# Kernel tuning notes

Measured on AMD Instinct MI355X. Metric: run time of the kernel, lower is better.

## Reference

```python
import jax, jax.numpy as jnp
import numpy as np

N_NODES = 100000   # n_user (70k) + m_item (30k)
N_EDGES = 2000000  # bidirectional user-item interaction edges
DIM = 64           # latent_dim = config['recdim']


def setup_inputs() -> dict:
    key = jax.random.key(0)
    k1, k2, k3, k4 = jax.random.split(key, 4)
    x = jax.random.normal(k1, (N_NODES, DIM), dtype=jnp.float32)
    edge_index = jax.random.randint(k2, (2, N_EDGES), 0, N_NODES, dtype=jnp.int32)
    # w_linears: Linear(2*D, D) per layer; stored as [in, out] so y = h @ W + b
    s = 1.0 / np.sqrt(2 * DIM)
    W0 = jax.random.normal(k3, (2 * DIM, DIM), dtype=jnp.float32) * s
    b0 = jnp.zeros((DIM,), dtype=jnp.float32)
    W1 = jax.random.normal(k4, (2 * DIM, DIM), dtype=jnp.float32) * s
    b1 = jnp.zeros((DIM,), dtype=jnp.float32)
    return {"x": x, "edge_index": edge_index, "W0": W0, "b0": b0, "W1": W1, "b1": b1}


def reference(x, edge_index, W0, b0, W1, b1):
    # SAGE-style: neighbor gather + mean aggregation + concat(self, agg) + per-layer linear
    n = x.shape[0]
    src = edge_index[0]  # message source nodes
    dst = edge_index[1]  # message destination nodes
    deg = jax.ops.segment_sum(jnp.ones(src.shape[0], x.dtype), dst, num_segments=n)
    inv_deg = (1.0 / jnp.maximum(deg, 1.0))[:, None]  # [N,1] mean normalizer

    h = x
    layers = ((W0, b0, True), (W1, b1, False))
    for W, b, apply_relu in layers:
        agg = jax.ops.segment_sum(h[src], dst, num_segments=n) * inv_deg  # [N,D] neighbor mean
        h = jnp.concatenate([h, agg], axis=1) @ W + b                      # [N,2D] @ [2D,D]
        if apply_relu:
            h = jax.nn.relu(h)
    return h
```

## Files before the change

### kernel.cpp

```cpp
#include <hip/hip_runtime.h>
#include <hip/hip_bf16.h>

#define N_NODES 100000
#define N_EDGES 2000000
#define DIM 64
#define NB 391
#define CAP 8192
#define PCAP 8192
#define EPB 4096
#define EPT 16
#define BIN_BLOCKS ((N_EDGES + EPB - 1) / EPB)
#define XCONV_BLOCKS (N_NODES * DIM / 4 / 256)

typedef __attribute__((ext_vector_type(8))) short short8;
typedef __attribute__((ext_vector_type(4))) float f32x4;
typedef __attribute__((ext_vector_type(2))) float f32x2;

__global__ __launch_bounds__(256) void binprep_kernel(const int* __restrict__ src,
                                                      const int* __restrict__ dst,
                                                      int* __restrict__ gbcur,
                                                      int* __restrict__ ebuf,
                                                      const float* __restrict__ x,
                                                      uint2* __restrict__ xb4,
                                                      int* __restrict__ xf8,
                                                      const float* __restrict__ W0,
                                                      const float* __restrict__ W1,
                                                      __hip_bfloat16* __restrict__ wfrag) {
    __shared__ int buf[EPB];
    __shared__ short bufb[EPB];
    __shared__ int a[512];
    __shared__ int lscan[NB], lcur[NB], gbase[NB];

    const int bid = blockIdx.x;
    if (bid >= BIN_BLOCKS) {
        const int pb = bid - BIN_BLOCKS;
        if (pb < XCONV_BLOCKS) {
            const int i = pb * 256 + threadIdx.x;
            const float4 v = ((const float4*)x)[i];
            __hip_bfloat162 p0 = __float22bfloat162_rn(make_float2(v.x, v.y));
            __hip_bfloat162 p1 = __float22bfloat162_rn(make_float2(v.z, v.w));
            uint2 ob;
            ob.x = *(unsigned int*)&p0;
            ob.y = *(unsigned int*)&p1;
            xb4[i] = ob;
            int w = __builtin_amdgcn_cvt_pk_fp8_f32(v.x, v.y, 0, false);
            w = __builtin_amdgcn_cvt_pk_fp8_f32(v.z, v.w, w, true);
            xf8[i] = w;
        } else {
            const int tid = (pb - XCONV_BLOCKS) * 256 + threadIdx.x;
            const int j    = tid & 7;
            const int lane = (tid >> 3) & 63;
            const int kc   = (tid >> 9) & 3;
            const int nt   = (tid >> 11) & 3;
            const int l    = tid >> 13;
            const int k = kc * 32 + (lane >> 4) * 8 + j;
            const int n = nt * 16 + (lane & 15);
            const float* W = l ? W1 : W0;
            wfrag[tid] = __float2bfloat16(W[k * 64 + n]);
        }
        return;
    }

    const int t = threadIdx.x;
    const int e0 = bid * EPB;
    const int cnt = min(EPB, N_EDGES - e0);

    for (int i = t; i < 512; i += 256) a[i] = 0;
    __syncthreads();

    int ls[EPT], ld[EPT];
    #pragma unroll
    for (int k = 0; k < EPT; ++k) {
        const int o = t + k * 256;
        if (o < cnt) {
            ls[k] = src[e0 + o];
            ld[k] = dst[e0 + o];
            atomicAdd(&a[ld[k] >> 8], 1);
        } else ld[k] = -1;
    }
    __syncthreads();

    #pragma unroll
    for (int d = 1; d < 512; d <<= 1) {
        const int idx = (t + 1) * 2 * d - 1;
        if (idx < 512) a[idx] += a[idx - d];
        __syncthreads();
    }
    if (t == 0) a[511] = 0;
    __syncthreads();
    #pragma unroll
    for (int d = 256; d >= 1; d >>= 1) {
        const int idx = (t + 1) * 2 * d - 1;
        if (idx < 512) {
            const int tmp = a[idx - d];
            a[idx - d] = a[idx];
            a[idx] += tmp;
        }
        __syncthreads();
    }
    for (int i = t; i < NB; i += 256) {
        const int c = a[i + 1] - a[i];
        lscan[i] = a[i];
        lcur[i]  = a[i];
        gbase[i] = c ? atomicAdd(&gbcur[i], c) : 0;
    }
    __syncthreads();

    #pragma unroll
    for (int k = 0; k < EPT; ++k) {
        if (ld[k] >= 0) {
            const int b = ld[k] >> 8;
            const int p = atomicAdd(&lcur[b], 1);
            buf[p]  = (ls[k] << 8) | (ld[k] & 255);
            bufb[p] = (short)b;
        }
    }
    __syncthreads();
    for (int i = t; i < cnt; i += 256) {
        const int pk = buf[i];
        const int b  = bufb[i];
        ebuf[b * CAP + gbase[b] + (i - lscan[b])] = pk;
    }
}

__global__ __launch_bounds__(256) void fillpass_kernel(const int* __restrict__ ebuf,
                                                       const int* __restrict__ gbcur,
                                                       int2* __restrict__ nodeinfo,
                                                       int* __restrict__ csr) {
    __shared__ int cnt[256];
    __shared__ int s[256];
    __shared__ int cur[256];
    const int b = blockIdx.x;
    const int t = threadIdx.x;
    const int nbase = b << 8;
    const int ecnt = gbcur[b];
    const int estart = b * CAP;

    cnt[t] = 0;
    __syncthreads();
    for (int i = t; i < ecnt; i += 256)
        atomicAdd(&cnt[ebuf[estart + i] & 255], 1);
    __syncthreads();

    const int deg  = cnt[t];
    const int pdeg = (deg + 7) & ~7;
    s[t] = pdeg;
    __syncthreads();
    #pragma unroll
    for (int off = 1; off < 256; off <<= 1) {
        int u = (t >= off) ? s[t - off] : 0;
        __syncthreads();
        s[t] += u;
        __syncthreads();
    }
    const int rp = b * PCAP + s[t] - pdeg;
    if (nbase + t < N_NODES) nodeinfo[nbase + t] = make_int2(rp, deg);
    cur[t] = rp;
    __syncthreads();

    for (int i = t; i < ecnt; i += 256) {
        const int pk = ebuf[estart + i];
        const int p = atomicAdd(&cur[pk & 255], 1);
        csr[p] = pk >> 8;
    }
    __syncthreads();
    for (int p = rp + deg; p < rp + pdeg; ++p)
        csr[p] = N_NODES;
}

__global__ __launch_bounds__(256) void gather_kernel(const uint2* __restrict__ f8tbl,
                                                     const int2* __restrict__ nodeinfo,
                                                     const int* __restrict__ csr,
                                                     uint4* __restrict__ agg16) {
    const int wave = threadIdx.x >> 6;
    const int lane = threadIdx.x & 63;
    const int node = blockIdx.x * 4 + wave;
    const int2 ni = nodeinfo[node];
    const int rp0 = ni.x;
    const int deg = ni.y;
    const int pcnt = (deg + 7) & ~7;
    const int o = lane >> 3;
    const int r = lane & 7;

    float a0 = 0.f, a1 = 0.f, a2 = 0.f, a3 = 0.f;
    float a4 = 0.f, a5 = 0.f, a6 = 0.f, a7 = 0.f;

    #define CONSUME(u)                                                        \
        {                                                                     \
            f32x2 f01 = __builtin_amdgcn_cvt_pk_f32_fp8((u).x, false);        \
            f32x2 f23 = __builtin_amdgcn_cvt_pk_f32_fp8((u).x, true);         \
            f32x2 f45 = __builtin_amdgcn_cvt_pk_f32_fp8((u).y, false);        \
            f32x2 f67 = __builtin_amdgcn_cvt_pk_f32_fp8((u).y, true);         \
            a0 += f01.x; a1 += f01.y; a2 += f23.x; a3 += f23.y;               \
            a4 += f45.x; a5 += f45.y; a6 += f67.x; a7 += f67.y;               \
        }

    for (int base = 0; base < pcnt; base += 64) {
        const int rem = min(pcnt - base, 64);
        const int idx = (lane < rem)
            ? __builtin_nontemporal_load(csr + rp0 + base + lane) : 0;
        int j = 0;
        for (; j + 32 <= rem; j += 32) {
            const int s0 = __shfl(idx, j + o);
            const int s1 = __shfl(idx, j + 8 + o);
            const int s2 = __shfl(idx, j + 16 + o);
            const int s3 = __shfl(idx, j + 24 + o);
            const uint2 u0 = f8tbl[(size_t)s0 * 8 + r];
            const uint2 u1 = f8tbl[(size_t)s1 * 8 + r];
            const uint2 u2 = f8tbl[(size_t)s2 * 8 + r];
            const uint2 u3 = f8tbl[(size_t)s3 * 8 + r];
            CONSUME(u0); CONSUME(u1); CONSUME(u2); CONSUME(u3);
        }
        for (; j < rem; j += 8) {
            const int s = __shfl(idx, j + o);
            const uint2 u = f8tbl[(size_t)s * 8 + r];
            CONSUME(u);
        }
    }
    #undef CONSUME

    #define RED(A) A += __shfl_xor(A, 8); A += __shfl_xor(A, 16); A += __shfl_xor(A, 32);
    RED(a0) RED(a1) RED(a2) RED(a3) RED(a4) RED(a5) RED(a6) RED(a7)
    #undef RED

    if (o == 0) {
        const float inv = 1.0f / fmaxf((float)deg, 1.0f);
        __hip_bfloat162 p0 = __float22bfloat162_rn(make_float2(a0 * inv, a1 * inv));
        __hip_bfloat162 p1 = __float22bfloat162_rn(make_float2(a2 * inv, a3 * inv));
        __hip_bfloat162 p2 = __float22bfloat162_rn(make_float2(a4 * inv, a5 * inv));
        __hip_bfloat162 p3 = __float22bfloat162_rn(make_float2(a6 * inv, a7 * inv));
        uint4 ov;
        ov.x = *(unsigned int*)&p0;
        ov.y = *(unsigned int*)&p1;
        ov.z = *(unsigned int*)&p2;
        ov.w = *(unsigned int*)&p3;
        agg16[(size_t)node * 8 + r] = ov;
    }
}

template <bool RELU, bool OUTF32, bool WRF8>
__global__ __launch_bounds__(256) void gemm_kernel(const unsigned short* __restrict__ hb,
                                                   const unsigned short* __restrict__ aggb,
                                                   const unsigned short* __restrict__ wfrag,
                                                   const float* __restrict__ bias,
                                                   float* __restrict__ outf,
                                                   unsigned short* __restrict__ outb,
                                                   unsigned char* __restrict__ outf8) {
    const int wave = threadIdx.x >> 6;
    const int lane = threadIdx.x & 63;
    const int m0 = (blockIdx.x * 4 + wave) * 16;
    const int quad = lane >> 4;
    const int lrow = lane & 15;
    const int m = min(m0 + lrow, N_NODES - 1);

    short8 bf[4][4];
    #pragma unroll
    for (int nt = 0; nt < 4; ++nt)
        #pragma unroll
        for (int kc = 0; kc < 4; ++kc)
            bf[nt][kc] = *(const short8*)(wfrag + (size_t)((nt * 4 + kc) * 64 + lane) * 8);

    f32x4 acc[4];
    #pragma unroll
    for (int nt = 0; nt < 4; ++nt) acc[nt] = f32x4{0.f, 0.f, 0.f, 0.f};

    #pragma unroll
    for (int kc = 0; kc < 4; ++kc) {
        const unsigned short* ap = (kc < 2)
            ? (hb   + (size_t)m * 64 + kc * 32 + quad * 8)
            : (aggb + (size_t)m * 64 + (kc - 2) * 32 + quad * 8);
        const short8 af = *(const short8*)ap;
        #pragma unroll
        for (int nt = 0; nt < 4; ++nt)
            acc[nt] = __builtin_amdgcn_mfma_f32_16x16x32_bf16(af, bf[nt][kc], acc[nt], 0, 0, 0);
    }

    #pragma unroll
    for (int nt = 0; nt < 4; ++nt) {
        const float bv = bias[nt * 16 + lrow];
        #pragma unroll
        for (int r = 0; r < 4; ++r) {
            const int mr = m0 + quad * 4 + r;
            if (mr < N_NODES) {
                float v = acc[nt][r] + bv;
                if (RELU) v = fmaxf(v, 0.f);
                const size_t off = (size_t)mr * 64 + nt * 16 + lrow;
                if (OUTF32) {
                    outf[off] = v;
                } else {
                    __hip_bfloat16 hv = __float2bfloat16(v);
                    outb[off] = *(unsigned short*)&hv;
                }
                if (WRF8) {
                    const int w8 = __builtin_amdgcn_cvt_pk_fp8_f32(v, v, 0, false);
                    outf8[off] = (unsigned char)(w8 & 0xff);
                }
            }
        }
    }
}

extern "C" void kernel_launch(void* const* d_in, const int* in_sizes, int n_in,
                              void* d_out, int out_size, void* d_ws, size_t ws_size,
                              hipStream_t stream) {
    const float* x  = (const float*)d_in[0];
    const int*   ei = (const int*)d_in[1];
    const float* W0 = (const float*)d_in[2];
    const float* b0 = (const float*)d_in[3];
    const float* W1 = (const float*)d_in[4];
    const float* b1 = (const float*)d_in[5];
    float* out = (float*)d_out;

    const int* src = ei;
    const int* dst = ei + N_EDGES;

    char* ws = (char*)d_ws;
    auto alloc = [&](size_t bytes) {
        char* p = ws;
        ws += (bytes + 255) & ~(size_t)255;
        return p;
    };
    int*  gbcur    = (int*)alloc((size_t)NB * 4);
    int2* nodeinfo = (int2*)alloc((size_t)N_NODES * 8);
    int*  ebuf     = (int*)alloc((size_t)NB * CAP * 4);
    int*  csr      = (int*)alloc((size_t)NB * PCAP * 4);
    unsigned short* xb   = (unsigned short*)alloc((size_t)N_NODES * DIM * 2);
    unsigned char*  xf8  = (unsigned char*)alloc((size_t)(N_NODES + 1) * DIM);
    unsigned short* aggb = (unsigned short*)alloc((size_t)N_NODES * DIM * 2);
    unsigned short* h1b  = (unsigned short*)alloc((size_t)N_NODES * DIM * 2);
    unsigned char*  h1f8 = (unsigned char*)alloc((size_t)(N_NODES + 1) * DIM);
    __hip_bfloat16* wfrag = (__hip_bfloat16*)alloc((size_t)2 * 8192 * 2);

    hipMemsetAsync(gbcur, 0, (size_t)NB * 4, stream);
    hipMemsetAsync(xf8  + (size_t)N_NODES * DIM, 0, DIM, stream);
    hipMemsetAsync(h1f8 + (size_t)N_NODES * DIM, 0, DIM, stream);

    binprep_kernel<<<BIN_BLOCKS + XCONV_BLOCKS + 64, 256, 0, stream>>>(
        src, dst, gbcur, ebuf, x, (uint2*)xb, (int*)xf8, W0, W1, wfrag);
    fillpass_kernel<<<NB, 256, 0, stream>>>(ebuf, gbcur, nodeinfo, csr);

    const int gemm_blocks = (N_NODES + 63) / 64;

    gather_kernel<<<N_NODES / 4, 256, 0, stream>>>((const uint2*)xf8, nodeinfo, csr,
                                                   (uint4*)aggb);
    gemm_kernel<true, false, true><<<gemm_blocks, 256, 0, stream>>>(
        xb, aggb, (const unsigned short*)wfrag, b0, nullptr, h1b, h1f8);

    gather_kernel<<<N_NODES / 4, 256, 0, stream>>>((const uint2*)h1f8, nodeinfo, csr,
                                                   (uint4*)aggb);
    gemm_kernel<false, true, false><<<gemm_blocks, 256, 0, stream>>>(
        h1b, aggb, (const unsigned short*)wfrag + 8192, b1, out, nullptr, nullptr);
}
```

Baseline: 244.7 us.

## Assign eight threads per node in gather with vectorized uint4 index loads

Changes the neighbor-mean gather from one 64-lane wave per node to an 8-thread group per node. Each group reads four CSR indices at once as a uint4, and the CSR padding is reduced from multiples of 8 to multiples of 4. This removes the wave-wide shuffles and the cross-lane reduction, and avoids idle lanes on low-degree nodes. The trade-off is possible load imbalance between the node groups that share a wave, and fewer independent loads in flight per node.

New measurement: 209.1 us. 14.5% less time.

```diff
diff --git a/kernel.cpp b/kernel.cpp
--- a/kernel.cpp
+++ b/kernel.cpp
@@ -143,7 +143,7 @@
     __syncthreads();
 
     const int deg  = cnt[t];
-    const int pdeg = (deg + 7) & ~7;
+    const int pdeg = (deg + 3) & ~3;
     s[t] = pdeg;
     __syncthreads();
     #pragma unroll
@@ -170,17 +170,15 @@
 
 __global__ __launch_bounds__(256) void gather_kernel(const uint2* __restrict__ f8tbl,
                                                      const int2* __restrict__ nodeinfo,
-                                                     const int* __restrict__ csr,
+                                                     const uint4* __restrict__ csr4,
                                                      uint4* __restrict__ agg16) {
-    const int wave = threadIdx.x >> 6;
-    const int lane = threadIdx.x & 63;
-    const int node = blockIdx.x * 4 + wave;
+    const int g = threadIdx.x >> 3;
+    const int r = threadIdx.x & 7;
+    const int node = blockIdx.x * 32 + g;
     const int2 ni = nodeinfo[node];
-    const int rp0 = ni.x;
+    const int c0 = ni.x >> 2;
     const int deg = ni.y;
-    const int pcnt = (deg + 7) & ~7;
-    const int o = lane >> 3;
-    const int r = lane & 7;
+    const int rounds = (deg + 3) >> 2;
 
     float a0 = 0.f, a1 = 0.f, a2 = 0.f, a3 = 0.f;
     float a4 = 0.f, a5 = 0.f, a6 = 0.f, a7 = 0.f;
@@ -195,47 +193,27 @@
             a4 += f45.x; a5 += f45.y; a6 += f67.x; a7 += f67.y;               \
         }
 
-    for (int base = 0; base < pcnt; base += 64) {
-        const int rem = min(pcnt - base, 64);
-        const int idx = (lane < rem)
-            ? __builtin_nontemporal_load(csr + rp0 + base + lane) : 0;
-        int j = 0;
-        for (; j + 32 <= rem; j += 32) {
-            const int s0 = __shfl(idx, j + o);
-            const int s1 = __shfl(idx, j + 8 + o);
-            const int s2 = __shfl(idx, j + 16 + o);
-            const int s3 = __shfl(idx, j + 24 + o);
-            const uint2 u0 = f8tbl[(size_t)s0 * 8 + r];
-            const uint2 u1 = f8tbl[(size_t)s1 * 8 + r];
-            const uint2 u2 = f8tbl[(size_t)s2 * 8 + r];
-            const uint2 u3 = f8tbl[(size_t)s3 * 8 + r];
-            CONSUME(u0); CONSUME(u1); CONSUME(u2); CONSUME(u3);
-        }
-        for (; j < rem; j += 8) {
-            const int s = __shfl(idx, j + o);
-            const uint2 u = f8tbl[(size_t)s * 8 + r];
-            CONSUME(u);
-        }
+    for (int t = 0; t < rounds; ++t) {
+        const uint4 id = csr4[c0 + t];
+        const uint2 u0 = f8tbl[(size_t)id.x * 8 + r];
+        const uint2 u1 = f8tbl[(size_t)id.y * 8 + r];
+        const uint2 u2 = f8tbl[(size_t)id.z * 8 + r];
+        const uint2 u3 = f8tbl[(size_t)id.w * 8 + r];
+        CONSUME(u0); CONSUME(u1); CONSUME(u2); CONSUME(u3);
     }
     #undef CONSUME
 
-    #define RED(A) A += __shfl_xor(A, 8); A += __shfl_xor(A, 16); A += __shfl_xor(A, 32);
-    RED(a0) RED(a1) RED(a2) RED(a3) RED(a4) RED(a5) RED(a6) RED(a7)
-    #undef RED
-
-    if (o == 0) {
-        const float inv = 1.0f / fmaxf((float)deg, 1.0f);
-        __hip_bfloat162 p0 = __float22bfloat162_rn(make_float2(a0 * inv, a1 * inv));
-        __hip_bfloat162 p1 = __float22bfloat162_rn(make_float2(a2 * inv, a3 * inv));
-        __hip_bfloat162 p2 = __float22bfloat162_rn(make_float2(a4 * inv, a5 * inv));
-        __hip_bfloat162 p3 = __float22bfloat162_rn(make_float2(a6 * inv, a7 * inv));
-        uint4 ov;
-        ov.x = *(unsigned int*)&p0;
-        ov.y = *(unsigned int*)&p1;
-        ov.z = *(unsigned int*)&p2;
-        ov.w = *(unsigned int*)&p3;
-        agg16[(size_t)node * 8 + r] = ov;
-    }
+    const float inv = 1.0f / fmaxf((float)deg, 1.0f);
+    __hip_bfloat162 p0 = __float22bfloat162_rn(make_float2(a0 * inv, a1 * inv));
+    __hip_bfloat162 p1 = __float22bfloat162_rn(make_float2(a2 * inv, a3 * inv));
+    __hip_bfloat162 p2 = __float22bfloat162_rn(make_float2(a4 * inv, a5 * inv));
+    __hip_bfloat162 p3 = __float22bfloat162_rn(make_float2(a6 * inv, a7 * inv));
+    uint4 ov;
+    ov.x = *(unsigned int*)&p0;
+    ov.y = *(unsigned int*)&p1;
+    ov.z = *(unsigned int*)&p2;
+    ov.w = *(unsigned int*)&p3;
+    agg16[(size_t)node * 8 + r] = ov;
 }
 
 template <bool RELU, bool OUTF32, bool WRF8>
@@ -341,13 +319,13 @@
 
     const int gemm_blocks = (N_NODES + 63) / 64;
 
-    gather_kernel<<<N_NODES / 4, 256, 0, stream>>>((const uint2*)xf8, nodeinfo, csr,
-                                                   (uint4*)aggb);
+    gather_kernel<<<N_NODES / 32, 256, 0, stream>>>((const uint2*)xf8, nodeinfo,
+                                                    (const uint4*)csr, (uint4*)aggb);
     gemm_kernel<true, false, true><<<gemm_blocks, 256, 0, stream>>>(
         xb, aggb, (const unsigned short*)wfrag, b0, nullptr, h1b, h1f8);
 
-    gather_kernel<<<N_NODES / 4, 256, 0, stream>>>((const uint2*)h1f8, nodeinfo, csr,
-                                                   (uint4*)aggb);
+    gather_kernel<<<N_NODES / 32, 256, 0, stream>>>((const uint2*)h1f8, nodeinfo,
+                                                    (const uint4*)csr, (uint4*)aggb);
     gemm_kernel<false, true, false><<<gemm_blocks, 256, 0, stream>>>(
         h1b, aggb, (const unsigned short*)wfrag + 8192, b1, out, nullptr, nullptr);
 }
```
